# Optimization experiments

Hardware: AMD Instinct MI355X
Metric: run time of the kernel (lower is better)

The kernel has to match this reference:

```python
import jax, jax.numpy as jnp
from jax import lax
import numpy as np
import math

N = 8
IN_CH = 3
EPS = 1e-6


def _dct_basis(n=N):
    # basis[u, i] = c(u) * cos(pi * u * (i + 0.5) / n)
    u = np.arange(n)
    i = np.arange(n)
    b = np.cos(np.pi * np.outer(u, i + 0.5) / n)
    c = np.full(n, math.sqrt(2.0 / n))
    c[0] = math.sqrt(1.0 / n)
    return b * c[:, None]


def _dct_conv_weight(n=N, in_ch=IN_CH):
    # weight[k = u*n + v, i, j] = basis[u,i] * basis[v,j]; grouped conv OIHW with I=1
    b = _dct_basis(n)
    w = np.einsum('ui,vj->uvij', b, b).reshape(n * n, 1, n, n).astype(np.float32)
    return np.concatenate([w] * in_ch, axis=0)  # [in_ch*n*n, 1, n, n]


def setup_inputs() -> dict:
    key = jax.random.key(0)
    k1, k2, k3 = jax.random.split(key, 3)
    B, C, H, W = 32, 3, 512, 512
    x = jax.random.uniform(k1, (B, C, H, W), dtype=jnp.float32)  # RGB in [0,1)
    # per-(sample, channel) stats; keep divisor d = max - min + eps > 1 so the
    # B-times repeated in-place normalization of the original stays finite
    max_ = 1.5 + jax.random.uniform(k2, (B, C * N * N, 1, 1), dtype=jnp.float32)
    min_ = 0.1 * jax.random.uniform(k3, (B, C * N * N, 1, 1), dtype=jnp.float32)
    ycbcr_w = jnp.asarray(
        [[0.299, 0.587, 0.114],
         [-0.169, -0.331, 0.5],
         [0.5, -0.419, -0.081]], dtype=jnp.float32)  # [out_c, in_c]
    dct_w = jnp.asarray(_dct_conv_weight())  # [192, 1, 8, 8]
    return {"x": x, "max_": max_, "min_": min_, "ycbcr_w": ycbcr_w, "dct_w": dct_w}


def reference(x, max_, min_, ycbcr_w, dct_w):
    # 1x1 RGB -> YCbCr conv == channel matmul
    ycbcr = jnp.einsum('oc,bchw->bohw', ycbcr_w, x)
    # grouped 8x8 stride-8 block-DCT conv: [B, 192, H/8, W/8]
    dct = lax.conv_general_dilated(
        ycbcr, dct_w, window_strides=(N, N), padding='VALID',
        feature_group_count=IN_CH,
        dimension_numbers=('NCHW', 'OIHW', 'NCHW'))
    # Original applies t = (t - min) / (max - min + eps) in-place B times per
    # sample (outer loop index i is unused but repeats the whole inner loop).
    d = max_ - min_ + EPS
    B = x.shape[0]
    out = lax.fori_loop(0, B, lambda i, t: (t - min_) / d, dct)
    return out
```

## Files before the change

### kernel.cpp

```cpp
#include <hip/hip_runtime.h>


#define HW 512
#define CHST (HW * HW)
#define NPAIR 6144
#define EPS 1e-6f

static constexpr float BASIS[8][8] = {
  { 0.35355339059327373f, 0.35355339059327373f, 0.35355339059327373f, 0.35355339059327373f,
    0.35355339059327373f, 0.35355339059327373f, 0.35355339059327373f, 0.35355339059327373f },
  { 0.49039264020161522f, 0.41573480615127262f, 0.27778511650980114f, 0.09754516100806412f,
   -0.09754516100806412f,-0.27778511650980114f,-0.41573480615127262f,-0.49039264020161522f },
  { 0.46193976625564337f, 0.19134171618254492f,-0.19134171618254492f,-0.46193976625564337f,
   -0.46193976625564337f,-0.19134171618254492f, 0.19134171618254492f, 0.46193976625564337f },
  { 0.41573480615127262f,-0.09754516100806412f,-0.49039264020161522f,-0.27778511650980114f,
    0.27778511650980114f, 0.49039264020161522f, 0.09754516100806412f,-0.41573480615127262f },
  { 0.35355339059327373f,-0.35355339059327373f,-0.35355339059327373f, 0.35355339059327373f,
    0.35355339059327373f,-0.35355339059327373f,-0.35355339059327373f, 0.35355339059327373f },
  { 0.27778511650980114f,-0.49039264020161522f, 0.09754516100806412f, 0.41573480615127262f,
   -0.41573480615127262f,-0.09754516100806412f, 0.49039264020161522f,-0.27778511650980114f },
  { 0.19134171618254492f,-0.46193976625564337f, 0.46193976625564337f,-0.19134171618254492f,
   -0.19134171618254492f, 0.46193976625564337f,-0.46193976625564337f, 0.19134171618254492f },
  { 0.09754516100806412f,-0.27778511650980114f, 0.41573480615127262f,-0.49039264020161522f,
    0.49039264020161522f,-0.41573480615127262f, 0.27778511650980114f,-0.09754516100806412f }
};

__global__ void precomp_norm(const float* __restrict__ max_,
                             const float* __restrict__ min_,
                             float* __restrict__ so) {
    int i = blockIdx.x * 256 + threadIdx.x;
    if (i >= NPAIR) return;
    float mn = min_[i], mx = max_[i];
    float d = mx - mn + EPS;
    float a = 1.0f / d;
    float a2 = a * a, a4 = a2 * a2, a8 = a4 * a4, a16 = a8 * a8, a32 = a16 * a16;
    float geo = a * (1.0f - a32) / (1.0f - a);
    so[2 * i]     = a32;
    so[2 * i + 1] = -mn * geo;
}

template <bool USE_WS>
__global__ __launch_bounds__(192)
void dct_kernel(const float* __restrict__ x,
                const float* __restrict__ ycbcr_w,
                const float* __restrict__ so,
                const float* __restrict__ max_,
                const float* __restrict__ min_,
                float* __restrict__ out) {
    const int b  = blockIdx.x >> 6;
    const int by = blockIdx.x & 63;
    const int c  = threadIdx.x >> 6;
    const int bx = threadIdx.x & 63;

    const float w0 = ycbcr_w[c * 3 + 0];
    const float w1 = ycbcr_w[c * 3 + 1];
    const float w2 = ycbcr_w[c * 3 + 2];

    const float* x0 = x + (size_t)(b * 3) * CHST + (by * 8) * HW + bx * 8;

    float tmp[8][8];
#pragma unroll
    for (int u = 0; u < 8; ++u)
#pragma unroll
        for (int j = 0; j < 8; ++j) tmp[u][j] = 0.0f;

#pragma unroll
    for (int i = 0; i < 8; ++i) {
        const float* r = x0 + i * HW;
        float R[8], G[8], Bl[8];
        *(float4*)(&R[0])  = *(const float4*)(r);
        *(float4*)(&R[4])  = *(const float4*)(r + 4);
        *(float4*)(&G[0])  = *(const float4*)(r + CHST);
        *(float4*)(&G[4])  = *(const float4*)(r + CHST + 4);
        *(float4*)(&Bl[0]) = *(const float4*)(r + 2 * CHST);
        *(float4*)(&Bl[4]) = *(const float4*)(r + 2 * CHST + 4);
        float y[8];
#pragma unroll
        for (int j = 0; j < 8; ++j)
            y[j] = fmaf(w0, R[j], fmaf(w1, G[j], w2 * Bl[j]));
#pragma unroll
        for (int u = 0; u < 8; ++u) {
            const float bu = BASIS[u][i];
#pragma unroll
            for (int j = 0; j < 8; ++j)
                tmp[u][j] = fmaf(bu, y[j], tmp[u][j]);
        }
    }

    const int obase = b * 192 + c * 64;
    float* op = out + ((size_t)obase * 64 + by) * 64 + bx;

#pragma unroll
    for (int u = 0; u < 8; ++u) {
#pragma unroll
        for (int v = 0; v < 8; ++v) {
            float acc = tmp[u][0] * BASIS[v][0];
#pragma unroll
            for (int j = 1; j < 8; ++j)
                acc = fmaf(tmp[u][j], BASIS[v][j], acc);
            const int k = u * 8 + v;
            float s, o;
            if (USE_WS) {
                s = so[(obase + k) * 2];
                o = so[(obase + k) * 2 + 1];
            } else {
                float mn = min_[obase + k], mx = max_[obase + k];
                float d  = mx - mn + EPS;
                float a  = 1.0f / d;
                float a2 = a * a, a4 = a2 * a2, a8 = a4 * a4, a16 = a8 * a8, a32 = a16 * a16;
                s = a32;
                o = -mn * (a * (1.0f - a32) / (1.0f - a));
            }
            op[(size_t)k * 4096] = fmaf(s, acc, o);
        }
    }
}

extern "C" void kernel_launch(void* const* d_in, const int* in_sizes, int n_in,
                              void* d_out, int out_size, void* d_ws, size_t ws_size,
                              hipStream_t stream) {
    const float* x    = (const float*)d_in[0];
    const float* max_ = (const float*)d_in[1];
    const float* min_ = (const float*)d_in[2];
    const float* yw   = (const float*)d_in[3];
    float* out = (float*)d_out;
    float* so  = (float*)d_ws;

    const bool use_ws = (ws_size >= (size_t)NPAIR * 2 * sizeof(float));
    if (use_ws) {
        precomp_norm<<<(NPAIR + 255) / 256, 256, 0, stream>>>(max_, min_, so);
        dct_kernel<true><<<32 * 64, 192, 0, stream>>>(x, yw, so, max_, min_, out);
    } else {
        dct_kernel<false><<<32 * 64, 192, 0, stream>>>(x, yw, nullptr, max_, min_, out);
    }
}
```

Measured before the change: 197.6 us.

## Process two block rows per workgroup with double-buffered row prefetch

Each workgroup now handles two 8x8 block rows instead of one, halving the grid to 1024 blocks. Row loads go into a two-slot register buffer that is issued two rows ahead, so global loads overlap the DCT accumulation. This adds register pressure from the 48-float buffer and cuts the number of resident waves, which may reduce latency hiding for a memory-bound kernel.

```diff
diff --git a/kernel.cpp b/kernel.cpp
--- a/kernel.cpp
+++ b/kernel.cpp
@@ -47,16 +47,34 @@
                 const float* __restrict__ max_,
                 const float* __restrict__ min_,
                 float* __restrict__ out) {
-    const int b  = blockIdx.x >> 6;
-    const int by = blockIdx.x & 63;
-    const int c  = threadIdx.x >> 6;
-    const int bx = threadIdx.x & 63;
+    const int g    = blockIdx.x;
+    const int b    = g >> 5;
+    const int byp  = g & 31;
+    const int c    = threadIdx.x >> 6;
+    const int bx   = threadIdx.x & 63;
 
     const float w0 = ycbcr_w[c * 3 + 0];
     const float w1 = ycbcr_w[c * 3 + 1];
     const float w2 = ycbcr_w[c * 3 + 2];
 
-    const float* x0 = x + (size_t)(b * 3) * CHST + (by * 8) * HW + bx * 8;
+    const float* xb = x + (size_t)(b * 3) * CHST + (size_t)(byp * 16) * HW + bx * 8;
+
+    float4 rb[2][6];
+
+    auto issue = [&](int slot, int r) {
+        const float* p = xb + (size_t)r * HW;
+        rb[slot][0] = *(const float4*)(p);
+        rb[slot][1] = *(const float4*)(p + 4);
+        rb[slot][2] = *(const float4*)(p + CHST);
+        rb[slot][3] = *(const float4*)(p + CHST + 4);
+        rb[slot][4] = *(const float4*)(p + 2 * CHST);
+        rb[slot][5] = *(const float4*)(p + 2 * CHST + 4);
+    };
+
+    issue(0, 0);
+    issue(1, 1);
+
+    const int obase = b * 192 + c * 64;
 
     float tmp[8][8];
 #pragma unroll
@@ -65,19 +83,22 @@
         for (int j = 0; j < 8; ++j) tmp[u][j] = 0.0f;
 
 #pragma unroll
-    for (int i = 0; i < 8; ++i) {
-        const float* r = x0 + i * HW;
-        float R[8], G[8], Bl[8];
-        *(float4*)(&R[0])  = *(const float4*)(r);
-        *(float4*)(&R[4])  = *(const float4*)(r + 4);
-        *(float4*)(&G[0])  = *(const float4*)(r + CHST);
-        *(float4*)(&G[4])  = *(const float4*)(r + CHST + 4);
-        *(float4*)(&Bl[0]) = *(const float4*)(r + 2 * CHST);
-        *(float4*)(&Bl[4]) = *(const float4*)(r + 2 * CHST + 4);
+    for (int r = 0; r < 16; ++r) {
+        const int sl = r & 1;
+        const int i  = r & 7;
+
         float y[8];
-#pragma unroll
-        for (int j = 0; j < 8; ++j)
-            y[j] = fmaf(w0, R[j], fmaf(w1, G[j], w2 * Bl[j]));
+        y[0] = fmaf(w0, rb[sl][0].x, fmaf(w1, rb[sl][2].x, w2 * rb[sl][4].x));
+        y[1] = fmaf(w0, rb[sl][0].y, fmaf(w1, rb[sl][2].y, w2 * rb[sl][4].y));
+        y[2] = fmaf(w0, rb[sl][0].z, fmaf(w1, rb[sl][2].z, w2 * rb[sl][4].z));
+        y[3] = fmaf(w0, rb[sl][0].w, fmaf(w1, rb[sl][2].w, w2 * rb[sl][4].w));
+        y[4] = fmaf(w0, rb[sl][1].x, fmaf(w1, rb[sl][3].x, w2 * rb[sl][5].x));
+        y[5] = fmaf(w0, rb[sl][1].y, fmaf(w1, rb[sl][3].y, w2 * rb[sl][5].y));
+        y[6] = fmaf(w0, rb[sl][1].z, fmaf(w1, rb[sl][3].z, w2 * rb[sl][5].z));
+        y[7] = fmaf(w0, rb[sl][1].w, fmaf(w1, rb[sl][3].w, w2 * rb[sl][5].w));
+
+        if (r + 2 < 16) issue(sl, r + 2);
+
 #pragma unroll
         for (int u = 0; u < 8; ++u) {
             const float bu = BASIS[u][i];
@@ -85,33 +106,41 @@
             for (int j = 0; j < 8; ++j)
                 tmp[u][j] = fmaf(bu, y[j], tmp[u][j]);
         }
-    }
 
-    const int obase = b * 192 + c * 64;
-    float* op = out + ((size_t)obase * 64 + by) * 64 + bx;
-
+        if (i == 7) {
+            const int by = byp * 2 + (r >> 3);
+            float* op = out + ((size_t)obase * 64 + by) * 64 + bx;
 #pragma unroll
-    for (int u = 0; u < 8; ++u) {
+            for (int u = 0; u < 8; ++u) {
 #pragma unroll
-        for (int v = 0; v < 8; ++v) {
-            float acc = tmp[u][0] * BASIS[v][0];
+                for (int v = 0; v < 8; ++v) {
+                    float acc = tmp[u][0] * BASIS[v][0];
 #pragma unroll
-            for (int j = 1; j < 8; ++j)
-                acc = fmaf(tmp[u][j], BASIS[v][j], acc);
-            const int k = u * 8 + v;
-            float s, o;
-            if (USE_WS) {
-                s = so[(obase + k) * 2];
-                o = so[(obase + k) * 2 + 1];
-            } else {
-                float mn = min_[obase + k], mx = max_[obase + k];
-                float d  = mx - mn + EPS;
-                float a  = 1.0f / d;
-                float a2 = a * a, a4 = a2 * a2, a8 = a4 * a4, a16 = a8 * a8, a32 = a16 * a16;
-                s = a32;
-                o = -mn * (a * (1.0f - a32) / (1.0f - a));
+                    for (int j = 1; j < 8; ++j)
+                        acc = fmaf(tmp[u][j], BASIS[v][j], acc);
+                    const int k = u * 8 + v;
+                    float s, o;
+                    if (USE_WS) {
+                        s = so[(obase + k) * 2];
+                        o = so[(obase + k) * 2 + 1];
+                    } else {
+                        float mn = min_[obase + k], mx = max_[obase + k];
+                        float d  = mx - mn + EPS;
+                        float a  = 1.0f / d;
+                        float a2 = a * a, a4 = a2 * a2, a8 = a4 * a4,
+                              a16 = a8 * a8, a32 = a16 * a16;
+                        s = a32;
+                        o = -mn * (a * (1.0f - a32) / (1.0f - a));
+                    }
+                    op[(size_t)k * 4096] = fmaf(s, acc, o);
+                }
             }
-            op[(size_t)k * 4096] = fmaf(s, acc, o);
+            if (r < 15) {
+#pragma unroll
+                for (int u = 0; u < 8; ++u)
+#pragma unroll
+                    for (int j = 0; j < 8; ++j) tmp[u][j] = 0.0f;
+            }
         }
     }
 }
@@ -129,8 +158,8 @@
     const bool use_ws = (ws_size >= (size_t)NPAIR * 2 * sizeof(float));
     if (use_ws) {
         precomp_norm<<<(NPAIR + 255) / 256, 256, 0, stream>>>(max_, min_, so);
-        dct_kernel<true><<<32 * 64, 192, 0, stream>>>(x, yw, so, max_, min_, out);
+        dct_kernel<true><<<32 * 32, 192, 0, stream>>>(x, yw, so, max_, min_, out);
     } else {
-        dct_kernel<false><<<32 * 64, 192, 0, stream>>>(x, yw, nullptr, max_, min_, out);
+        dct_kernel<false><<<32 * 32, 192, 0, stream>>>(x, yw, nullptr, max_, min_, out);
     }
 }
```

New measurement: 198.4 us. About the same (+0.4%).
